# Performance work log

Measured on AMD Instinct MI355X. Metric: run time of the kernel, lower is better.

## Reference

```python
import jax, jax.numpy as jnp
import numpy as np

N = 100000      # num nodes
E = 1600000     # num edges
IN = 128        # in_channels
OUT = 128       # out_channels
K = 2           # num_k_hops


def setup_inputs() -> dict:
    key = jax.random.key(0)
    k1, k2, k3 = jax.random.split(key, 3)
    x = jax.random.normal(k1, (N, IN), dtype=jnp.float32)
    edge_index = jax.random.randint(k2, (2, E), 0, N, dtype=jnp.int32)
    # Linear(in, out) params, kaiming-uniform-ish scale
    W = jax.random.normal(k3, (OUT, IN), dtype=jnp.float32) * (1.0 / np.sqrt(IN))
    b = jnp.zeros((OUT,), dtype=jnp.float32)
    return {"x": x, "edge_index": edge_index, "W": W, "b": b}


def reference(x, edge_index, W, b):
    n = x.shape[0]
    # gcn_norm: add self-loops, symmetric normalization deg^-1/2 A_hat deg^-1/2
    loop = jnp.arange(n, dtype=edge_index.dtype)
    row = jnp.concatenate([edge_index[0], loop])  # source j
    col = jnp.concatenate([edge_index[1], loop])  # target i
    deg = jax.ops.segment_sum(jnp.ones_like(col, dtype=x.dtype), col, num_segments=n)
    dinv = jnp.where(deg > 0, jax.lax.rsqrt(deg), jnp.zeros_like(deg))
    norm = dinv[row] * dinv[col]  # [E+N]

    def hop(h, _):
        # out[i] = sum_{(j->i)} norm_ij * h[j]  (gather + scatter-add SpMM)
        msg = norm[:, None] * h[row]
        return jax.ops.segment_sum(msg, col, num_segments=n), None

    h, _ = jax.lax.scan(hop, x, None, length=K)
    # final linear projection (SGConv.lin)
    return h @ W.T + b
```

## Files before the change

kernel.cpp:

```cpp
#include <hip/hip_runtime.h>

#define CAP 64
#define NPB 256
#define NPB_SHIFT 8
#define CAPB 4864
#define EPB 8192
#define MAXB 512

typedef __attribute__((ext_vector_type(8))) short short8v;
typedef __attribute__((ext_vector_type(4))) float f32x4;

__device__ __forceinline__ unsigned f2bf(float f) {
  unsigned u = __float_as_uint(f);
  u += 0x7fffu + ((u >> 16) & 1u);
  return u >> 16;
}
__device__ __forceinline__ float bflo(unsigned u) { return __uint_as_float(u << 16); }
__device__ __forceinline__ float bfhi(unsigned u) { return __uint_as_float(u & 0xffff0000u); }

__global__ __launch_bounds__(256) void k_binA(const int* __restrict__ row,
                                              const int* __restrict__ col,
                                              int* __restrict__ gcur,
                                              unsigned int* __restrict__ binned,
                                              int E, int nb) {
  __shared__ int lcnt[MAXB];
  int tid = threadIdx.x;
  for (int i = tid; i < nb; i += 256) lcnt[i] = 0;
  __syncthreads();
  int e0 = blockIdx.x * EPB;
#pragma unroll
  for (int it = 0; it < EPB / 256; ++it) {
    int e = e0 + it * 256 + tid;
    if (e < E) atomicAdd(&lcnt[col[e] >> NPB_SHIFT], 1);
  }
  __syncthreads();
  for (int b = tid; b < nb; b += 256) {
    int c = lcnt[b];
    lcnt[b] = (c > 0) ? atomicAdd(&gcur[b], c) : 0;
  }
  __syncthreads();
#pragma unroll
  for (int it = 0; it < EPB / 256; ++it) {
    int e = e0 + it * 256 + tid;
    if (e < E) {
      int c = col[e];
      int s = row[e];
      int b = c >> NPB_SHIFT;
      int pos = atomicAdd(&lcnt[b], 1);
      if (pos < (b + 1) * CAPB)
        binned[pos] = ((unsigned)s << NPB_SHIFT) | (unsigned)(c & (NPB - 1));
    }
  }
}

__global__ __launch_bounds__(256) void k_binB(const unsigned int* __restrict__ binned,
                                              const int* __restrict__ gcur,
                                              int* __restrict__ counts,
                                              float* __restrict__ dinv,
                                              int* __restrict__ srcbuf,
                                              int N) {
  __shared__ int cur[NPB];
  int tid = threadIdx.x;
  int b = blockIdx.x;
  cur[tid] = 0;
  __syncthreads();
  int cnt = gcur[b] - b * CAPB;
  if (cnt > CAPB) cnt = CAPB;
  const unsigned int* bp = binned + (size_t)b * CAPB;
  int nb0 = b << NPB_SHIFT;
  for (int e = tid; e < cnt; e += 256) {
    unsigned p = bp[e];
    int li = p & (NPB - 1);
    int s = (int)(p >> NPB_SHIFT);
    int r = atomicAdd(&cur[li], 1);
    if (r < CAP) srcbuf[((size_t)(nb0 + li) << 6) + r] = s;
  }
  __syncthreads();
  int node = nb0 + tid;
  if (node < N) {
    int c = cur[tid];
    counts[node] = c;
    dinv[node] = rsqrtf((float)c + 1.0f);
  }
}

__global__ void k_init(int* __restrict__ gcur, int nb) {
  int i = blockIdx.x * blockDim.x + threadIdx.x;
  if (i < nb) gcur[i] = i * CAPB;
}

__global__ __launch_bounds__(256) void k_prescale(const float2* __restrict__ x2,
                                                  const float* __restrict__ dinv,
                                                  unsigned* __restrict__ xb,
                                                  int n64) {
  int i = blockIdx.x * blockDim.x + threadIdx.x;
  if (i >= n64) return;
  float d = dinv[i >> 6];
  float2 v = x2[i];
  xb[i] = f2bf(v.x * d) | (f2bf(v.y * d) << 16);
}

template <int MODE>
__global__ __launch_bounds__(256) void k_hop(
    const unsigned* __restrict__ hin, unsigned* __restrict__ hout,
    const int* __restrict__ srcbuf, const int* __restrict__ counts,
    const float* __restrict__ dinv, int n) {
  int wave = __builtin_amdgcn_readfirstlane((int)(threadIdx.x >> 6));
  int lane = threadIdx.x & 63;
  int node = blockIdx.x * 4 + wave;
  if (node >= n) return;
  int cnt = counts[node];
  if (cnt > CAP) cnt = CAP;
  float di = dinv[node];
  unsigned su = hin[((size_t)node << 6) + lane];
  float ax = bflo(su);
  float ay = bfhi(su);
  const int* sp = srcbuf + ((size_t)node << 6);
  int e = 0;
  for (; e + 8 <= cnt; e += 8) {
    int sid[8];
    unsigned v[8];
#pragma unroll
    for (int u = 0; u < 8; ++u) sid[u] = sp[e + u];
#pragma unroll
    for (int u = 0; u < 8; ++u) v[u] = hin[((size_t)sid[u] << 6) + lane];
#pragma unroll
    for (int u = 0; u < 8; ++u) {
      ax += bflo(v[u]);
      ay += bfhi(v[u]);
    }
  }
  for (; e < cnt; ++e) {
    unsigned v0 = hin[((size_t)sp[e] << 6) + lane];
    ax += bflo(v0);
    ay += bfhi(v0);
  }
  float s = (MODE == 1) ? di * di : di;
  hout[((size_t)node << 6) + lane] = f2bf(ax * s) | (f2bf(ay * s) << 16);
}

__global__ __launch_bounds__(256) void k_gemm_mfma(
    const unsigned* __restrict__ h2b,
    const float* __restrict__ W,
    const float* __restrict__ bias,
    float* __restrict__ out, int n) {
  __shared__ short Wl[128 * 128];
  int tid = threadIdx.x;
  const float4* Wg4 = (const float4*)W;
#pragma unroll
  for (int it = 0; it < 8; ++it) {
    int idx = tid + (it << 8);
    int c = idx >> 4;
    int j = idx & 15;
    float4 a = Wg4[c * 32 + j * 2];
    float4 bq = Wg4[c * 32 + j * 2 + 1];
    short8v s;
    s[0] = (short)f2bf(a.x);  s[1] = (short)f2bf(a.y);
    s[2] = (short)f2bf(a.z);  s[3] = (short)f2bf(a.w);
    s[4] = (short)f2bf(bq.x); s[5] = (short)f2bf(bq.y);
    s[6] = (short)f2bf(bq.z); s[7] = (short)f2bf(bq.w);
    int eo = (j << 3) ^ ((c & 7) << 3);
    *(short8v*)&Wl[(c << 7) + eo] = s;
  }
  __syncthreads();

  int wv = __builtin_amdgcn_readfirstlane((int)(tid >> 6));
  int lane = tid & 63;
  int tiles = (n + 15) >> 4;
  int tile = blockIdx.x * 4 + wv;
  if (tile >= tiles) return;
  int row0 = tile << 4;
  int r = lane & 15, g = lane >> 4;

  int arow = row0 + r;
  if (arow >= n) arow = n - 1;
  const short* hrow = (const short*)(h2b + ((size_t)arow << 6));
  short8v A0 = *(const short8v*)&hrow[g * 8];
  short8v A1 = *(const short8v*)&hrow[g * 8 + 32];
  short8v A2 = *(const short8v*)&hrow[g * 8 + 64];
  short8v A3 = *(const short8v*)&hrow[g * 8 + 96];

#pragma unroll
  for (int ct = 0; ct < 8; ++ct) {
    int c = (ct << 4) + r;
    int sw = (c & 7) << 3;
    const short* wrow = &Wl[c << 7];
    short8v B0 = *(const short8v*)&wrow[(g * 8) ^ sw];
    short8v B1 = *(const short8v*)&wrow[(g * 8 + 32) ^ sw];
    short8v B2 = *(const short8v*)&wrow[(g * 8 + 64) ^ sw];
    short8v B3 = *(const short8v*)&wrow[(g * 8 + 96) ^ sw];
    f32x4 acc = {0.f, 0.f, 0.f, 0.f};
    acc = __builtin_amdgcn_mfma_f32_16x16x32_bf16(A0, B0, acc, 0, 0, 0);
    acc = __builtin_amdgcn_mfma_f32_16x16x32_bf16(A1, B1, acc, 0, 0, 0);
    acc = __builtin_amdgcn_mfma_f32_16x16x32_bf16(A2, B2, acc, 0, 0, 0);
    acc = __builtin_amdgcn_mfma_f32_16x16x32_bf16(A3, B3, acc, 0, 0, 0);
    float bb = bias[c];
#pragma unroll
    for (int q = 0; q < 4; ++q) {
      int rr = row0 + g * 4 + q;
      if (rr < n) out[(size_t)rr * 128 + c] = acc[q] + bb;
    }
  }
}

extern "C" void kernel_launch(void* const* d_in, const int* in_sizes, int n_in,
                              void* d_out, int out_size, void* d_ws, size_t ws_size,
                              hipStream_t stream) {
  const float* x = (const float*)d_in[0];
  const int* ei = (const int*)d_in[1];
  const float* W = (const float*)d_in[2];
  const float* b = (const float*)d_in[3];
  int N = in_sizes[0] / 128;
  int E = in_sizes[1] / 2;
  float* out = (float*)d_out;

  char* ws = (char*)d_ws;
  int* counts = (int*)ws;
  float* dinv = (float*)(ws + (512u << 10));
  int* gcur = (int*)(ws + (960u << 10));
  int* srcbuf = (int*)(ws + (1u << 20));
  unsigned* xb = (unsigned*)(ws + (27u << 20));
  unsigned* h2b = xb;
  unsigned* h1b = (unsigned*)(ws + (53u << 20));
  unsigned int* binned = (unsigned int*)(ws + (53u << 20));

  int nb = (N + NPB - 1) >> NPB_SHIFT;
  int blocksA = (E + EPB - 1) / EPB;
  int tiles = (N + 15) >> 4;

  k_init<<<(nb + 255) / 256, 256, 0, stream>>>(gcur, nb);
  k_binA<<<blocksA, 256, 0, stream>>>(ei, ei + E, gcur, binned, E, nb);
  k_binB<<<nb, 256, 0, stream>>>(binned, gcur, counts, dinv, srcbuf, N);
  k_prescale<<<(N * 64 + 255) / 256, 256, 0, stream>>>((const float2*)x, dinv, xb, N * 64);
  k_hop<1><<<(N + 3) / 4, 256, 0, stream>>>(xb, h1b, srcbuf, counts, dinv, N);
  k_hop<2><<<(N + 3) / 4, 256, 0, stream>>>(h1b, h2b, srcbuf, counts, dinv, N);
  k_gemm_mfma<<<(tiles + 3) / 4, 256, 0, stream>>>(h2b, W, b, out, N);
}
```

Before: 214.6 us.

## Vectorize hop gathers to 16-byte loads with padded neighbor lists

The hop kernel now has each lane load a uint4 slice of a neighbor row, so one wave gathers four neighbors at once. The four partial sums are then combined with cross-lane shuffles. The binning stage appends the self-loop to each node's source list and pads the list to a multiple of 8 with a dummy node index whose row is zeroed by memset, which removes the separate self load and the scalar tail loop. The aim is fewer, wider memory instructions and more loads in flight per wave. The cost is wasted loads on padding entries, an extra shuffle reduction per node, and a source-list capacity lowered by one entry.

```diff
diff --git a/kernel.cpp b/kernel.cpp
--- a/kernel.cpp
+++ b/kernel.cpp
@@ -73,13 +73,18 @@
     int li = p & (NPB - 1);
     int s = (int)(p >> NPB_SHIFT);
     int r = atomicAdd(&cur[li], 1);
-    if (r < CAP) srcbuf[((size_t)(nb0 + li) << 6) + r] = s;
+    if (r < CAP - 1) srcbuf[((size_t)(nb0 + li) << 6) + r] = s;
   }
   __syncthreads();
   int node = nb0 + tid;
   if (node < N) {
     int c = cur[tid];
-    counts[node] = c;
+    int mlen = (c < CAP - 1) ? c : (CAP - 1);
+    int* myp = srcbuf + ((size_t)node << 6);
+    myp[mlen] = node;
+    int cntp = (mlen + 1 + 7) & ~7;
+    for (int p2 = mlen + 1; p2 < cntp; ++p2) myp[p2] = N;
+    counts[node] = cntp;
     dinv[node] = rsqrtf((float)c + 1.0f);
   }
 }
@@ -100,6 +105,12 @@
   xb[i] = f2bf(v.x * d) | (f2bf(v.y * d) << 16);
 }
 
+#define ACC8(v)                          \
+  a[0] += bflo((v).x); a[1] += bfhi((v).x); \
+  a[2] += bflo((v).y); a[3] += bfhi((v).y); \
+  a[4] += bflo((v).z); a[5] += bfhi((v).z); \
+  a[6] += bflo((v).w); a[7] += bfhi((v).w);
+
 template <int MODE>
 __global__ __launch_bounds__(256) void k_hop(
     const unsigned* __restrict__ hin, unsigned* __restrict__ hout,
@@ -109,41 +120,47 @@
   int lane = threadIdx.x & 63;
   int node = blockIdx.x * 4 + wave;
   if (node >= n) return;
-  int cnt = counts[node];
-  if (cnt > CAP) cnt = CAP;
+  int cntp = counts[node];
   float di = dinv[node];
-  unsigned su = hin[((size_t)node << 6) + lane];
-  float ax = bflo(su);
-  float ay = bfhi(su);
+  int g = lane >> 4;
+  int m = lane & 15;
+  const uint4* h4 = (const uint4*)hin;
   const int* sp = srcbuf + ((size_t)node << 6);
+  float a[8];
+#pragma unroll
+  for (int i = 0; i < 8; ++i) a[i] = 0.f;
   int e = 0;
-  for (; e + 8 <= cnt; e += 8) {
-    int sid[8];
-    unsigned v[8];
-#pragma unroll
-    for (int u = 0; u < 8; ++u) sid[u] = sp[e + u];
-#pragma unroll
-    for (int u = 0; u < 8; ++u) v[u] = hin[((size_t)sid[u] << 6) + lane];
-#pragma unroll
-    for (int u = 0; u < 8; ++u) {
-      ax += bflo(v[u]);
-      ay += bfhi(v[u]);
-    }
-  }
-  for (; e < cnt; ++e) {
-    unsigned v0 = hin[((size_t)sp[e] << 6) + lane];
-    ax += bflo(v0);
-    ay += bfhi(v0);
+  for (; e + 16 <= cntp; e += 16) {
+    int s0 = sp[e + g];
+    int s1 = sp[e + 4 + g];
+    int s2 = sp[e + 8 + g];
+    int s3 = sp[e + 12 + g];
+    uint4 v0 = h4[((size_t)s0 << 4) + m];
+    uint4 v1 = h4[((size_t)s1 << 4) + m];
+    uint4 v2 = h4[((size_t)s2 << 4) + m];
+    uint4 v3 = h4[((size_t)s3 << 4) + m];
+    ACC8(v0); ACC8(v1); ACC8(v2); ACC8(v3);
+  }
+  if (e < cntp) {
+    int s0 = sp[e + g];
+    int s1 = sp[e + 4 + g];
+    uint4 v0 = h4[((size_t)s0 << 4) + m];
+    uint4 v1 = h4[((size_t)s1 << 4) + m];
+    ACC8(v0); ACC8(v1);
+  }
+#pragma unroll
+  for (int i = 0; i < 8; ++i) {
+    a[i] += __shfl_xor(a[i], 32);
+    a[i] += __shfl_xor(a[i], 16);
   }
   float s = (MODE == 1) ? di * di : di;
-  hout[((size_t)node << 6) + lane] = f2bf(ax * s) | (f2bf(ay * s) << 16);
+  unsigned o = f2bf(a[2 * g] * s) | (f2bf(a[2 * g + 1] * s) << 16);
+  hout[((size_t)node << 6) + (m << 2) + g] = o;
 }
 
 __global__ __launch_bounds__(256) void k_gemm_mfma(
-    const unsigned* __restrict__ h2b,
-    const float* __restrict__ W,
-    const float* __restrict__ bias,
-    float* __restrict__ out, int n) {
+    const unsigned* __restrict__ h2b, const float* __restrict__ W,
+    const float* __restrict__ bias, float* __restrict__ out, int n) {
   __shared__ short Wl[128 * 128];
   int tid = threadIdx.x;
   const float4* Wg4 = (const float4*)W;
@@ -228,6 +245,9 @@
   int blocksA = (E + EPB - 1) / EPB;
   int tiles = (N + 15) >> 4;
 
+  hipMemsetAsync(xb + ((size_t)N << 6), 0, 256, stream);
+  hipMemsetAsync(h1b + ((size_t)N << 6), 0, 256, stream);
+
   k_init<<<(nb + 255) / 256, 256, 0, stream>>>(gcur, nb);
   k_binA<<<blocksA, 256, 0, stream>>>(ei, ei + E, gcur, binned, E, nb);
   k_binB<<<nb, 256, 0, stream>>>(binned, gcur, counts, dinv, srcbuf, N);
```

Result: faster. 209.9 us (-2.2%).
